# Kernel optimization log

Measured on AMD Instinct MI355X. Metric: run time of the kernel, lower is better.

Reference implementation:

```python
import jax, jax.numpy as jnp
import numpy as np

D_MODEL, D_STATE, D_CONV, EXPAND = 1024, 16, 4, 2
D_INNER = EXPAND * D_MODEL            # 2048
DT_RANK = int(np.ceil(D_MODEL / 16))  # 64
B, L = 2, 2048


def _dt_bias(key):
    # matches torch init: dt ~ exp(U(log dt_min, log dt_max)), inv via softplus inverse
    dt = jnp.exp(jax.random.uniform(key, (D_INNER,)) * (np.log(0.1) - np.log(0.001)) + np.log(0.001))
    dt = jnp.clip(dt, 1e-4, None)
    return dt + jnp.log(-jnp.expm1(-dt))


def _A_log():
    return jnp.log(jnp.tile(jnp.arange(1, D_STATE + 1, dtype=jnp.float32)[None, :], (D_INNER, 1)))


def setup_inputs() -> dict:
    key = jax.random.key(0)
    ks = jax.random.split(key, 16)
    n = lambda k, shape, s=0.02: jax.random.normal(k, shape, jnp.float32) * s
    return {
        "hidden_states": jax.random.normal(ks[0], (B, L, D_MODEL), jnp.float32),
        "in_proj_w": n(ks[1], (2 * D_INNER, D_MODEL)),
        "conv_w": n(ks[2], (D_INNER, 1, D_CONV), 0.2),
        "conv_b": jnp.zeros((D_INNER,), jnp.float32),
        "x_proj_w": n(ks[3], (DT_RANK + 2 * D_STATE, D_INNER)),
        "dt_proj_w": n(ks[4], (D_INNER, DT_RANK), 0.1),
        "dt_proj_b": _dt_bias(ks[5]),
        "A_log": _A_log(),
        "D": jnp.ones((D_INNER,), jnp.float32),
        "conv_w_b": n(ks[6], (D_INNER, 1, D_CONV), 0.2),
        "conv_b_b": jnp.zeros((D_INNER,), jnp.float32),
        "x_proj_w_b": n(ks[7], (DT_RANK + 2 * D_STATE, D_INNER)),
        "dt_proj_w_b": n(ks[8], (D_INNER, DT_RANK), 0.1),
        "dt_proj_b_b": _dt_bias(ks[9]),
        "A_b_log": _A_log(),
        "D_b": jnp.ones((D_INNER,), jnp.float32),
        "out_proj_w": n(ks[10], (D_MODEL, D_INNER)),
    }


def _silu(x):
    return x * jax.nn.sigmoid(x)


def _causal_dw_conv(x, w, b):
    # x: (B, Di, L); w: (Di, 1, K) depthwise; left-pad K-1 => causal, output length L
    y = jax.lax.conv_general_dilated(
        x, w, window_strides=(1,), padding=[(D_CONV - 1, 0)],
        dimension_numbers=("NCH", "OIH", "NCH"), feature_group_count=x.shape[1])
    return y + b[None, :, None]


def _mamba_branch(xz, conv_w, conv_b, x_proj_w, dt_proj_w, dt_proj_b, A_log, Dp):
    # xz: (B, 2*Di, L) -> y: (B, Di, L); selective scan (mamba_inner_fn_no_out_proj)
    x, z = jnp.split(xz, 2, axis=1)
    x = _silu(_causal_dw_conv(x, conv_w, conv_b))                       # (B,Di,L)
    x_dbl = jnp.einsum('rd,bdl->brl', x_proj_w, x)
    dt_r, Bc, Cc = jnp.split(x_dbl, [DT_RANK, DT_RANK + D_STATE], axis=1)
    delta = jax.nn.softplus(jnp.einsum('dr,brl->bdl', dt_proj_w, dt_r) + dt_proj_b[None, :, None])
    A = -jnp.exp(A_log)                                                 # (Di,N)

    def step(h, inp):
        d_t, u_t, b_t, c_t = inp   # (B,Di),(B,Di),(B,N),(B,N)
        h = h * jnp.exp(d_t[..., None] * A) + (d_t * u_t)[..., None] * b_t[:, None, :]
        return h, jnp.einsum('bdn,bn->bd', h, c_t)

    h0 = jnp.zeros((x.shape[0], D_INNER, D_STATE), x.dtype)
    xs = (jnp.moveaxis(delta, 2, 0), jnp.moveaxis(x, 2, 0),
          jnp.moveaxis(Bc, 2, 0), jnp.moveaxis(Cc, 2, 0))
    _, ys = jax.lax.scan(step, h0, xs)                                  # (L,B,Di)
    y = jnp.moveaxis(ys, 0, 2) + x * Dp[None, :, None]
    return y * _silu(z)


def reference(hidden_states, in_proj_w, conv_w, conv_b, x_proj_w, dt_proj_w, dt_proj_b,
              A_log, D, conv_w_b, conv_b_b, x_proj_w_b, dt_proj_w_b, dt_proj_b_b,
              A_b_log, D_b, out_proj_w):
    # bimamba_type == 'v2': forward scan + flipped backward scan, summed, then out_proj (no biases)
    xz = jnp.einsum('ed,bld->bel', in_proj_w, hidden_states)            # (B, 2*Di, L)
    out_f = _mamba_branch(xz, conv_w, conv_b, x_proj_w, dt_proj_w, dt_proj_b, A_log, D)
    out_r = _mamba_branch(xz[..., ::-1], conv_w_b, conv_b_b, x_proj_w_b,
                          dt_proj_w_b, dt_proj_b_b, A_b_log, D_b)[..., ::-1]
    y = out_f + out_r                                                   # (B,Di,L)
    return jnp.einsum('me,bel->blm', out_proj_w, y)                     # (B,L,D)
```

## Files before the change

kernel.cpp:

```cpp
#include <hip/hip_runtime.h>
#include <hip/hip_bf16.h>
#include <math.h>


#define L_SEQ  2048
#define B_SZ   2
#define DM     1024
#define DI     2048
#define NST    16
#define RTOT   96
#define DTR    64
#define NTOT   (B_SZ * L_SEQ)
#define ETOT   (2 * DI)
#define SPLK   8
#define CHTMAX 64

#define LOG2E  1.44269504088896340736f

#define OFF_X    ((size_t)0)
#define OFF_ZT   (OFF_X   + (size_t)DI * NTOT)
#define OFF_XCF  (OFF_ZT  + (size_t)DI * NTOT)
#define OFF_XCB  (OFF_XCF + (size_t)DI * NTOT)
#define OFF_DLTB (OFF_XCB + (size_t)DI * NTOT)
#define OFF_XDF  (OFF_DLTB + (size_t)DI * NTOT)
#define OFF_XDB  (OFF_XDF + (size_t)RTOT * NTOT)
#define OFF_SS   (OFF_XDB + (size_t)RTOT * NTOT)
#define OFF_HL   (OFF_SS  + (size_t)4 * 32 * DI)
#define OFF_YGTF (OFF_HL  + (size_t)4 * 32 * NST * DI)
#define OFF_YGTB (OFF_YGTF + (size_t)NTOT * DI / 2)
#define OFF_XDT16F (OFF_YGTB + (size_t)NTOT * DI / 2)
#define OFF_XDT16B (OFF_XDT16F + (size_t)NTOT * DTR / 2)
#define OFF_DTW16F (OFF_XDT16B + (size_t)NTOT * DTR / 2)
#define OFF_DTW16B (OFF_DTW16F + (size_t)DI * DTR / 2)
#define WS_FLOATS  (OFF_DTW16B + (size_t)DI * DTR / 2)
#define WS64_FLOATS (WS_FLOATS + (size_t)4 * 64 * DI + (size_t)4 * 64 * NST * DI)

typedef __bf16 bf16x8 __attribute__((ext_vector_type(8)));
typedef float  floatx4 __attribute__((ext_vector_type(4)));

__device__ __forceinline__ float silu_f(float x) {
    return x / (1.f + __expf(-x));
}

__device__ __forceinline__ void gl2lds16(const __bf16* g, __bf16* l) {
    __builtin_amdgcn_global_load_lds(
        (const __attribute__((address_space(1))) unsigned int*)g,
        (__attribute__((address_space(3))) unsigned int*)l, 16, 0, 0);
}

template<int MT, bool TRANS, bool SPLITZ>
__global__ __launch_bounds__(256)
void gemm_bf16(const __bf16* __restrict__ A, const __bf16* __restrict__ B,
               float* __restrict__ C, float* __restrict__ C2,
               int M, int N, int K)
{
    static_assert(MT == 64 || MT == 128, "vmcnt literals assume MT in {64,128}");
    __shared__ __attribute__((aligned(16))) __bf16 As[2][MT * 32];
    __shared__ __attribute__((aligned(16))) __bf16 Bs[2][128 * 32];
    const int tid  = threadIdx.x;
    const int m0   = blockIdx.y * MT;
    const int n0   = blockIdx.x * 128;
    const int lane = tid & 63;
    const int wave = tid >> 6;
    const int wy   = wave >> 1, wx = wave & 1;
    const int lr   = lane & 15;
    const int q    = lane >> 4;
    constexpr int MF = MT / 32;

    floatx4 acc[MF][4];
#pragma unroll
    for (int i = 0; i < MF; ++i)
#pragma unroll
        for (int j = 0; j < 4; ++j) acc[i][j] = (floatx4)(0.0f);

    const int rl = lane >> 2;
    const int cp = lane & 3;
    const int sw = (q ^ ((lr >> 2) & 3)) * 8;

    auto stage = [&](int s, int k0) {
#pragma unroll
        for (int is = 0; is < MT / 64; ++is) {
            int r0  = wave * (MT / 4) + is * 16;
            int row = r0 + rl;
            int c   = cp ^ ((row >> 2) & 3);
            gl2lds16(A + (size_t)(m0 + row) * K + k0 + c * 8, &As[s][r0 * 32]);
        }
#pragma unroll
        for (int is = 0; is < 2; ++is) {
            int r0  = wave * 32 + is * 16;
            int row = r0 + rl;
            int c   = cp ^ ((row >> 2) & 3);
            gl2lds16(B + (size_t)(n0 + row) * K + k0 + c * 8, &Bs[s][r0 * 32]);
        }
    };

    stage(0, 0);
    int cur = 0;
    for (int k0 = 0; k0 < K; k0 += 32) {
        if (k0 + 32 < K) {
            stage(cur ^ 1, k0 + 32);
            if constexpr (MT == 128) {
                asm volatile("s_waitcnt vmcnt(4)" ::: "memory");
            } else {
                asm volatile("s_waitcnt vmcnt(3)" ::: "memory");
            }
        } else {
            asm volatile("s_waitcnt vmcnt(0)" ::: "memory");
        }
        __builtin_amdgcn_s_barrier();

        bf16x8 af[MF], bfr[4];
#pragma unroll
        for (int i = 0; i < MF; ++i)
            af[i] = *(const bf16x8*)&As[cur][(wy * (MT / 2) + i * 16 + lr) * 32 + sw];
#pragma unroll
        for (int j = 0; j < 4; ++j)
            bfr[j] = *(const bf16x8*)&Bs[cur][(wx * 64 + j * 16 + lr) * 32 + sw];
#pragma unroll
        for (int i = 0; i < MF; ++i)
#pragma unroll
            for (int j = 0; j < 4; ++j)
                acc[i][j] = __builtin_amdgcn_mfma_f32_16x16x32_bf16(
                    af[i], bfr[j], acc[i][j], 0, 0, 0);
        __builtin_amdgcn_s_barrier();
        cur ^= 1;
    }

    const int mb = m0 + wy * (MT / 2);
    const int nb = n0 + wx * 64;
#pragma unroll
    for (int i = 0; i < MF; ++i) {
#pragma unroll
        for (int j = 0; j < 4; ++j) {
            int gn  = nb + j * 16 + lr;
            int gm0 = mb + i * 16 + q * 4;
            if constexpr (SPLITZ) {
                if (m0 < DI) {
#pragma unroll
                    for (int r = 0; r < 4; ++r)
                        C[(size_t)(gm0 + r) * N + gn] = acc[i][j][r];
                } else {
                    *(floatx4*)&C2[(size_t)gn * DI + (gm0 - DI)] = acc[i][j];
                }
            } else if constexpr (TRANS) {
                *(floatx4*)&C[(size_t)gn * M + gm0] = acc[i][j];
            } else {
#pragma unroll
                for (int r = 0; r < 4; ++r)
                    C[(size_t)(gm0 + r) * N + gn] = acc[i][j][r];
            }
        }
    }
}

__global__ __launch_bounds__(256)
void dtproj_mfma(const __bf16* __restrict__ Af, const __bf16* __restrict__ Ab,
                 const __bf16* __restrict__ Bwf, const __bf16* __restrict__ Bwb,
                 const float* __restrict__ bif, const float* __restrict__ bib,
                 float* __restrict__ outf, float* __restrict__ outb)
{
    __shared__ __attribute__((aligned(16))) __bf16 As[2][128 * 32];
    __shared__ __attribute__((aligned(16))) __bf16 Bs[2][128 * 32];
    const int br = blockIdx.z;
    const __bf16* A  = br ? Ab : Af;
    const __bf16* B  = br ? Bwb : Bwf;
    const float*  bi = br ? bib : bif;
    float*        C  = br ? outb : outf;

    const int tid  = threadIdx.x;
    const int m0   = blockIdx.y * 128;
    const int n0   = blockIdx.x * 128;
    const int lane = tid & 63;
    const int wave = tid >> 6;
    const int wy   = wave >> 1, wx = wave & 1;
    const int lr   = lane & 15;
    const int q    = lane >> 4;

    floatx4 acc[4][4];
#pragma unroll
    for (int i = 0; i < 4; ++i)
#pragma unroll
        for (int j = 0; j < 4; ++j) acc[i][j] = (floatx4)(0.0f);

    const int rl = lane >> 2;
    const int cp = lane & 3;
    const int sw = (q ^ ((lr >> 2) & 3)) * 8;

#pragma unroll
    for (int t = 0; t < 2; ++t) {
        int k0 = t * 32;
#pragma unroll
        for (int is = 0; is < 2; ++is) {
            int r0  = wave * 32 + is * 16;
            int row = r0 + rl;
            int c   = cp ^ ((row >> 2) & 3);
            gl2lds16(A + (size_t)(m0 + row) * DTR + k0 + c * 8, &As[t][r0 * 32]);
            gl2lds16(B + (size_t)(n0 + row) * DTR + k0 + c * 8, &Bs[t][r0 * 32]);
        }
    }

#pragma unroll
    for (int t = 0; t < 2; ++t) {
        if (t == 0) asm volatile("s_waitcnt vmcnt(4)" ::: "memory");
        else        asm volatile("s_waitcnt vmcnt(0)" ::: "memory");
        __builtin_amdgcn_s_barrier();

        bf16x8 af[4], bfr[4];
#pragma unroll
        for (int i = 0; i < 4; ++i)
            af[i] = *(const bf16x8*)&As[t][(wy * 64 + i * 16 + lr) * 32 + sw];
#pragma unroll
        for (int j = 0; j < 4; ++j)
            bfr[j] = *(const bf16x8*)&Bs[t][(wx * 64 + j * 16 + lr) * 32 + sw];
#pragma unroll
        for (int i = 0; i < 4; ++i)
#pragma unroll
            for (int j = 0; j < 4; ++j)
                acc[i][j] = __builtin_amdgcn_mfma_f32_16x16x32_bf16(
                    af[i], bfr[j], acc[i][j], 0, 0, 0);
    }

    const int mb = m0 + wy * 64;
    const int nb = n0 + wx * 64;
    float bj[4];
#pragma unroll
    for (int j = 0; j < 4; ++j) bj[j] = bi[nb + j * 16 + lr];
#pragma unroll
    for (int i = 0; i < 4; ++i) {
#pragma unroll
        for (int r = 0; r < 4; ++r) {
            int gm = mb + i * 16 + q * 4 + r;
#pragma unroll
            for (int j = 0; j < 4; ++j) {
                int gn = nb + j * 16 + lr;
                float x = acc[i][j][r] + bj[j];
                float o = (x > 20.f) ? x : __logf(1.f + __expf(x));
                C[(size_t)gm * DI + gn] = o;
            }
        }
    }
}

__global__ __launch_bounds__(256)
void cvt_bf16_k(const float* __restrict__ in, __bf16* __restrict__ out)
{
    const size_t i = ((size_t)blockIdx.x * 256 + threadIdx.x) * 8;
    float4 a = *(const float4*)(in + i);
    float4 b = *(const float4*)(in + i + 4);
    bf16x8 p;
    p[0]=(__bf16)a.x; p[1]=(__bf16)a.y; p[2]=(__bf16)a.z; p[3]=(__bf16)a.w;
    p[4]=(__bf16)b.x; p[5]=(__bf16)b.y; p[6]=(__bf16)b.z; p[7]=(__bf16)b.w;
    *(bf16x8*)(out + i) = p;
}

__global__ __launch_bounds__(256)
void addbf16_k(const __bf16* __restrict__ a, const __bf16* __restrict__ b,
               __bf16* __restrict__ o)
{
    const size_t i = ((size_t)blockIdx.x * 256 + threadIdx.x) * 8;
    bf16x8 x = *(const bf16x8*)(a + i);
    bf16x8 y = *(const bf16x8*)(b + i);
    bf16x8 s;
#pragma unroll
    for (int e = 0; e < 8; ++e) s[e] = (__bf16)((float)x[e] + (float)y[e]);
    *(bf16x8*)(o + i) = s;
}

__global__ __launch_bounds__(256)
void gemm_k3(const float* __restrict__ A, const float* __restrict__ Bm,
             float* __restrict__ C, int M, int N, int K)
{
    __shared__ float As[16][132];
    __shared__ float Bs[16][132];
    const int tid = threadIdx.x;
    const int n0 = blockIdx.x * 128;
    const int m0 = blockIdx.y * 128;
    int ksz  = K / (int)gridDim.z;
    int kbeg = blockIdx.z * ksz;
    int kend = kbeg + ksz;
    C += (size_t)blockIdx.z * M * N;
    const int tx = tid & 15, ty = tid >> 4;

    float acc[8][8];
#pragma unroll
    for (int i = 0; i < 8; ++i)
#pragma unroll
        for (int j = 0; j < 8; ++j) acc[i][j] = 0.f;

    for (int k0 = kbeg; k0 < kend; k0 += 16) {
#pragma unroll
        for (int it = 0; it < 2; ++it) {
            int i = tid + it * 256;
            int m = i >> 2, kq = i & 3;
            float4 v = make_float4(0.f, 0.f, 0.f, 0.f);
            int gm = m0 + m;
            if (gm < M) v = *(const float4*)(A + (size_t)gm * K + (k0 + kq * 4));
            As[kq * 4 + 0][m] = v.x; As[kq * 4 + 1][m] = v.y;
            As[kq * 4 + 2][m] = v.z; As[kq * 4 + 3][m] = v.w;
        }
#pragma unroll
        for (int it = 0; it < 2; ++it) {
            int i = tid + it * 256;
            int n = i >> 2, kq = i & 3;
            float4 v = *(const float4*)(Bm + (size_t)(n0 + n) * K + (k0 + kq * 4));
            Bs[kq * 4 + 0][n] = v.x; Bs[kq * 4 + 1][n] = v.y;
            Bs[kq * 4 + 2][n] = v.z; Bs[kq * 4 + 3][n] = v.w;
        }
        __syncthreads();
#pragma unroll
        for (int kk = 0; kk < 16; ++kk) {
            float av[8], bv[8];
            *(float4*)&av[0] = *(const float4*)&As[kk][ty * 8];
            *(float4*)&av[4] = *(const float4*)&As[kk][ty * 8 + 4];
            *(float4*)&bv[0] = *(const float4*)&Bs[kk][tx * 8];
            *(float4*)&bv[4] = *(const float4*)&Bs[kk][tx * 8 + 4];
#pragma unroll
            for (int i = 0; i < 8; ++i)
#pragma unroll
                for (int j = 0; j < 8; ++j)
                    acc[i][j] = fmaf(av[i], bv[j], acc[i][j]);
        }
        __syncthreads();
    }

#pragma unroll
    for (int i = 0; i < 8; ++i) {
        int gm = m0 + ty * 8 + i;
        if (gm < M) {
            float* cp = C + (size_t)gm * N + n0 + tx * 8;
            *(float4*)cp       = make_float4(acc[i][0], acc[i][1], acc[i][2], acc[i][3]);
            *(float4*)(cp + 4) = make_float4(acc[i][4], acc[i][5], acc[i][6], acc[i][7]);
        }
    }
}

__global__ __launch_bounds__(256)
void reduce8t_k(const float* __restrict__ P, float* __restrict__ out,
                __bf16* __restrict__ out2, size_t stride)
{
    const size_t i4 = ((size_t)blockIdx.x * 256 + threadIdx.x) * 4;
    float4 s = *(const float4*)(P + i4);
#pragma unroll
    for (int z = 1; z < SPLK; ++z) {
        float4 v = *(const float4*)(P + (size_t)z * stride + i4);
        s.x += v.x; s.y += v.y; s.z += v.z; s.w += v.w;
    }
    *(float4*)(out + i4) = s;
    const int r = (int)(i4 >> 12);
    if (r < DTR) {
        const int n = (int)(i4 & (NTOT - 1));
        out2[(size_t)(n + 0) * DTR + r] = (__bf16)s.x;
        out2[(size_t)(n + 1) * DTR + r] = (__bf16)s.y;
        out2[(size_t)(n + 2) * DTR + r] = (__bf16)s.z;
        out2[(size_t)(n + 3) * DTR + r] = (__bf16)s.w;
    }
}

__global__ __launch_bounds__(256)
void conv_k(const float* __restrict__ x,
            const float* __restrict__ wf, const float* __restrict__ bf,
            const float* __restrict__ wb, const float* __restrict__ bb,
            float* __restrict__ xcf, float* __restrict__ xcb)
{
    __shared__ float xs[70 * 65];
    const int tid = threadIdx.x;
    const int d0 = blockIdx.x * 64;
    const int n0 = blockIdx.y * 64;
    const int b  = n0 >> 11;
    const int l0 = n0 & (L_SEQ - 1);
    const size_t bbase = (size_t)b << 11;

    for (int i = tid; i < 64 * 70; i += 256) {
        int r = i / 70, c = i % 70;
        int l = l0 - 3 + c;
        float v = 0.f;
        if (l >= 0 && l < L_SEQ) v = x[(size_t)(d0 + r) * NTOT + bbase + l];
        xs[c * 65 + r] = v;
    }
    __syncthreads();

    const int dd = tid & 63;
    const int lq = tid >> 6;
    const int d  = d0 + dd;
    const float w0 = wf[d * 4 + 0], w1 = wf[d * 4 + 1];
    const float w2 = wf[d * 4 + 2], w3 = wf[d * 4 + 3];
    const float v0 = wb[d * 4 + 0], v1 = wb[d * 4 + 1];
    const float v2 = wb[d * 4 + 2], v3 = wb[d * 4 + 3];
    const float bfv = bf[d], bbv = bb[d];

    for (int lr = 0; lr < 64; lr += 4) {
        const int lo = lr + lq;
        const int l  = l0 + lo;
        float x0 = xs[(lo + 0) * 65 + dd];
        float x1 = xs[(lo + 1) * 65 + dd];
        float x2 = xs[(lo + 2) * 65 + dd];
        float x3 = xs[(lo + 3) * 65 + dd];
        float x4 = xs[(lo + 4) * 65 + dd];
        float x5 = xs[(lo + 5) * 65 + dd];
        float x6 = xs[(lo + 6) * 65 + dd];
        float xf = bfv + w0 * x0 + w1 * x1 + w2 * x2 + w3 * x3;
        xcf[((size_t)bbase + l) * DI + d] = silu_f(xf);
        float xb = bbv + v3 * x3 + v2 * x4 + v1 * x5 + v0 * x6;
        xcb[((size_t)bbase + (L_SEQ - 1 - l)) * DI + d] = silu_f(xb);
    }
}

__global__ __launch_bounds__(256)
void scan_part1(const float* __restrict__ xcf, const float* __restrict__ xcb,
                const float* __restrict__ xdf, const float* __restrict__ xdb,
                const float* __restrict__ dltf, const float* __restrict__ dltb,
                const float* __restrict__ Alog_f, const float* __restrict__ Alog_b,
                float* __restrict__ SS, float* __restrict__ HL,
                int nch, int csh)
{
    __shared__ float Bsh[NST][CHTMAX];
    const int cht = 1 << csh;
    const int tid = threadIdx.x;
    const int d  = blockIdx.x * 256 + tid;
    const int c  = blockIdx.y;
    const int bb = blockIdx.z;
    const int b  = bb & 1;
    const int br = bb >> 1;

    const float* u    = br ? xcb : xcf;
    const float* dl   = br ? dltb : dltf;
    const float* xd   = br ? xdb : xdf;
    const float* Alog = br ? Alog_b : Alog_f;

    const size_t nbase = (size_t)b * L_SEQ + (size_t)c * cht;
    const float* bcB = xd + (size_t)DTR * NTOT + nbase;

    for (int i = tid; i < NST * cht; i += 256) {
        int n = i >> csh;
        int t = i & (cht - 1);
        Bsh[n][t] = bcB[(size_t)n * NTOT + t];
    }

    float Arow[NST], h[NST];
#pragma unroll
    for (int n = 0; n < NST; ++n) {
        Arow[n] = -__expf(Alog[d * NST + n]) * LOG2E;
        h[n] = 0.f;
    }
    float S = 0.f;

    const float* up = u  + nbase * DI + d;
    const float* dp = dl + nbase * DI + d;

    __syncthreads();

    float dva[4], uva[4], dvb[4], uvb[4];
#pragma unroll
    for (int k = 0; k < 4; ++k) {
        dva[k] = dp[(size_t)k * DI];
        uva[k] = up[(size_t)k * DI];
    }
#pragma unroll
    for (int k = 0; k < 4; ++k) {
        dvb[k] = dp[(size_t)(4 + k) * DI];
        uvb[k] = up[(size_t)(4 + k) * DI];
    }

    for (int tr = 0; tr < cht; tr += 4) {
        float dvn[4], uvn[4];
#pragma unroll
        for (int k = 0; k < 4; ++k) {
            dvn[k] = dp[(size_t)(tr + 8 + k) * DI];
            uvn[k] = up[(size_t)(tr + 8 + k) * DI];
        }
        S += (dva[0] + dva[1]) + (dva[2] + dva[3]);
        float du[4] = { dva[0]*uva[0], dva[1]*uva[1], dva[2]*uva[2], dva[3]*uva[3] };
#pragma unroll
        for (int n = 0; n < NST; ++n) {
            float4 Bn = *(const float4*)&Bsh[n][tr];
            float hn = h[n];
            float An = Arow[n];
            hn = hn * __builtin_amdgcn_exp2f(dva[0] * An) + du[0] * Bn.x;
            hn = hn * __builtin_amdgcn_exp2f(dva[1] * An) + du[1] * Bn.y;
            hn = hn * __builtin_amdgcn_exp2f(dva[2] * An) + du[2] * Bn.z;
            hn = hn * __builtin_amdgcn_exp2f(dva[3] * An) + du[3] * Bn.w;
            h[n] = hn;
        }
#pragma unroll
        for (int k = 0; k < 4; ++k) {
            dva[k] = dvb[k]; uva[k] = uvb[k];
            dvb[k] = dvn[k]; uvb[k] = uvn[k];
        }
    }
    SS[((size_t)bb * nch + c) * DI + d] = S;
#pragma unroll
    for (int n = 0; n < NST; ++n)
        HL[(((size_t)bb * nch + c) * NST + n) * DI + d] = h[n];
}

__global__ __launch_bounds__(256)
void scan_part2(const float* __restrict__ SS, float* HL,
                const float* __restrict__ Alog_f, const float* __restrict__ Alog_b,
                int nch)
{
    const int d  = blockIdx.x * 256 + threadIdx.x;
    const int n  = blockIdx.y;
    const int bb = blockIdx.z;
    const int br = bb >> 1;
    const float* Alog = br ? Alog_b : Alog_f;
    const float A = -__expf(Alog[d * NST + n]) * LOG2E;

    float H = 0.f;
    for (int c = 0; c < nch; ++c) {
        const size_t si = ((size_t)bb * nch + c) * DI + d;
        const size_t hi = (((size_t)bb * nch + c) * NST + n) * DI + d;
        float hl = HL[hi];
        HL[hi] = H;
        H = __builtin_amdgcn_exp2f(SS[si] * A) * H + hl;
    }
}

__global__ __launch_bounds__(256)
void scan_part3(const float* __restrict__ zt,
                const float* __restrict__ xcf, const float* __restrict__ xcb,
                const float* __restrict__ xdf, const float* __restrict__ xdb,
                const float* __restrict__ dltf, const float* __restrict__ dltb,
                const float* __restrict__ HIN,
                __bf16* __restrict__ ygtf, __bf16* __restrict__ ygtb,
                const float* __restrict__ Alog_f, const float* __restrict__ Alog_b,
                const float* __restrict__ Df, const float* __restrict__ Db,
                int nch, int csh)
{
    __shared__ float BCs[2 * NST][CHTMAX];
    const int cht = 1 << csh;
    const int tid = threadIdx.x;
    const int d  = blockIdx.x * 256 + tid;
    const int c  = blockIdx.y;
    const int bb = blockIdx.z;
    const int b  = bb & 1;
    const int br = bb >> 1;

    const float* u    = br ? xcb : xcf;
    const float* dl   = br ? dltb : dltf;
    const float* xd   = br ? xdb : xdf;
    const float* Alog = br ? Alog_b : Alog_f;
    const float* Dv   = br ? Db : Df;
    __bf16*      ygt  = br ? ygtb : ygtf;

    const size_t nbase = (size_t)b * L_SEQ + (size_t)c * cht;
    const float* bcB = xd + (size_t)DTR * NTOT + nbase;

    for (int i = tid; i < 2 * NST * cht; i += 256) {
        int n = i >> csh;
        int t = i & (cht - 1);
        BCs[n][t] = bcB[(size_t)n * NTOT + t];
    }

    float Arow[NST], h[NST];
#pragma unroll
    for (int n = 0; n < NST; ++n) {
        Arow[n] = -__expf(Alog[d * NST + n]) * LOG2E;
        h[n] = HIN[(((size_t)bb * nch + c) * NST + n) * DI + d];
    }
    const float Dp = Dv[d];

    const float* up = u  + nbase * DI + d;
    const float* dp = dl + nbase * DI + d;
    const int    bL = b * L_SEQ;
    const int    t0 = c * cht;

    __syncthreads();

    float dva[4], uva[4], dvb[4], uvb[4];
#pragma unroll
    for (int k = 0; k < 4; ++k) {
        dva[k] = dp[(size_t)k * DI];
        uva[k] = up[(size_t)k * DI];
    }
#pragma unroll
    for (int k = 0; k < 4; ++k) {
        dvb[k] = dp[(size_t)(4 + k) * DI];
        uvb[k] = up[(size_t)(4 + k) * DI];
    }
    int   ncur[4];
    float zcur[4];
#pragma unroll
    for (int k = 0; k < 4; ++k) {
        int t = t0 + k;
        ncur[k] = br ? (bL + (L_SEQ - 1 - t)) : (bL + t);
        zcur[k] = zt[(ptrdiff_t)ncur[k] * DI + d];
    }

    for (int tr = 0; tr < cht; tr += 4) {
        float dvn[4], uvn[4], znx[4];
        int   nnx[4];
#pragma unroll
        for (int k = 0; k < 4; ++k) {
            dvn[k] = dp[(size_t)(tr + 8 + k) * DI];
            uvn[k] = up[(size_t)(tr + 8 + k) * DI];
        }
#pragma unroll
        for (int k = 0; k < 4; ++k) {
            int t = t0 + tr + 4 + k;
            nnx[k] = br ? (bL + (L_SEQ - 1 - t)) : (bL + t);
            znx[k] = zt[(ptrdiff_t)nnx[k] * DI + d];
        }

        float du[4] = { dva[0]*uva[0], dva[1]*uva[1], dva[2]*uva[2], dva[3]*uva[3] };
        float y[4] = { 0.f, 0.f, 0.f, 0.f };
#pragma unroll
        for (int n = 0; n < NST; ++n) {
            float4 Bn = *(const float4*)&BCs[n][tr];
            float4 Cn = *(const float4*)&BCs[NST + n][tr];
            float hn = h[n];
            float An = Arow[n];
            hn = hn * __builtin_amdgcn_exp2f(dva[0] * An) + du[0] * Bn.x;  y[0] = fmaf(hn, Cn.x, y[0]);
            hn = hn * __builtin_amdgcn_exp2f(dva[1] * An) + du[1] * Bn.y;  y[1] = fmaf(hn, Cn.y, y[1]);
            hn = hn * __builtin_amdgcn_exp2f(dva[2] * An) + du[2] * Bn.z;  y[2] = fmaf(hn, Cn.z, y[2]);
            hn = hn * __builtin_amdgcn_exp2f(dva[3] * An) + du[3] * Bn.w;  y[3] = fmaf(hn, Cn.w, y[3]);
            h[n] = hn;
        }
#pragma unroll
        for (int k = 0; k < 4; ++k) {
            float yo = (y[k] + uva[k] * Dp) * silu_f(zcur[k]);
            ygt[(size_t)ncur[k] * DI + d] = (__bf16)yo;
        }
#pragma unroll
        for (int k = 0; k < 4; ++k) {
            dva[k] = dvb[k]; uva[k] = uvb[k];
            dvb[k] = dvn[k]; uvb[k] = uvn[k];
            ncur[k] = nnx[k]; zcur[k] = znx[k];
        }
    }
}

extern "C" void kernel_launch(void* const* d_in, const int* in_sizes, int n_in,
                              void* d_out, int out_size, void* d_ws, size_t ws_size,
                              hipStream_t stream)
{
    const float* hid     = (const float*)d_in[0];
    const float* inw     = (const float*)d_in[1];
    const float* convw   = (const float*)d_in[2];
    const float* convb   = (const float*)d_in[3];
    const float* xpw     = (const float*)d_in[4];
    const float* dtw     = (const float*)d_in[5];
    const float* dtb     = (const float*)d_in[6];
    const float* Alog    = (const float*)d_in[7];
    const float* Dv      = (const float*)d_in[8];
    const float* convw_b = (const float*)d_in[9];
    const float* convb_b = (const float*)d_in[10];
    const float* xpw_b   = (const float*)d_in[11];
    const float* dtw_b   = (const float*)d_in[12];
    const float* dtb_b   = (const float*)d_in[13];
    const float* Alog_b  = (const float*)d_in[14];
    const float* Dv_b    = (const float*)d_in[15];
    const float* outw    = (const float*)d_in[16];
    float* out = (float*)d_out;
    float* ws  = (float*)d_ws;

    if (ws_size < WS_FLOATS * sizeof(float)) return;

    const bool big = ws_size >= WS64_FLOATS * sizeof(float);
    const int  nch = big ? 64 : 32;
    const int  csh = big ? 5 : 6;

    float*  X    = ws + OFF_X;
    float*  ZT   = ws + OFF_ZT;
    float*  XCF  = ws + OFF_XCF;
    float*  XCB  = ws + OFF_XCB;
    float*  DLTB = ws + OFF_DLTB;
    float*  XDF  = ws + OFF_XDF;
    float*  XDB  = ws + OFF_XDB;
    float*  SS   = big ? (ws + WS_FLOATS) : (ws + OFF_SS);
    float*  HLb  = SS + (size_t)4 * nch * DI;
    __bf16* YGTF = (__bf16*)(ws + OFF_YGTF);
    __bf16* YGTB = (__bf16*)(ws + OFF_YGTB);
    float*  PF   = ws + OFF_YGTF;
    float*  PB   = ws + OFF_YGTB;
    float*  DLTF = X;
    __bf16* IW16 = (__bf16*)(ws + OFF_SS);
    __bf16* HD16 = IW16 + (size_t)ETOT * DM;
    __bf16* OW16 = (__bf16*)(ws + OFF_XCB);
    __bf16* YGS  = (__bf16*)(ws + OFF_XCF);
    __bf16* XDT16F = (__bf16*)(ws + OFF_XDT16F);
    __bf16* XDT16B = (__bf16*)(ws + OFF_XDT16B);
    __bf16* DTW16F = (__bf16*)(ws + OFF_DTW16F);
    __bf16* DTW16B = (__bf16*)(ws + OFF_DTW16B);

    dim3 blk(256);
    cvt_bf16_k<<<dim3(ETOT * DM / 2048), blk, 0, stream>>>(inw, IW16);
    cvt_bf16_k<<<dim3(NTOT * DM / 2048), blk, 0, stream>>>(hid, HD16);
    cvt_bf16_k<<<dim3(DI * DTR / 2048), blk, 0, stream>>>(dtw, DTW16F);
    cvt_bf16_k<<<dim3(DI * DTR / 2048), blk, 0, stream>>>(dtw_b, DTW16B);
    gemm_bf16<128, false, true><<<dim3(32, 32), blk, 0, stream>>>(
        IW16, HD16, X, ZT, ETOT, NTOT, DM);
    conv_k<<<dim3(32, 64), blk, 0, stream>>>(X, convw, convb, convw_b, convb_b, XCF, XCB);
    gemm_k3<<<dim3(32, 1, SPLK), blk, 0, stream>>>(xpw, XCF, PF, RTOT, NTOT, DI);
    gemm_k3<<<dim3(32, 1, SPLK), blk, 0, stream>>>(xpw_b, XCB, PB, RTOT, NTOT, DI);
    reduce8t_k<<<dim3(RTOT * NTOT / 1024), blk, 0, stream>>>(PF, XDF, XDT16F, (size_t)RTOT * NTOT);
    reduce8t_k<<<dim3(RTOT * NTOT / 1024), blk, 0, stream>>>(PB, XDB, XDT16B, (size_t)RTOT * NTOT);
    dtproj_mfma<<<dim3(DI / 128, NTOT / 128, 2), blk, 0, stream>>>(
        XDT16F, XDT16B, DTW16F, DTW16B, dtb, dtb_b, DLTF, DLTB);
    scan_part1<<<dim3(DI / 256, nch, 4), blk, 0, stream>>>(
        XCF, XCB, XDF, XDB, DLTF, DLTB, Alog, Alog_b, SS, HLb, nch, csh);
    scan_part2<<<dim3(DI / 256, NST, 4), blk, 0, stream>>>(
        SS, HLb, Alog, Alog_b, nch);
    scan_part3<<<dim3(DI / 256, nch, 4), blk, 0, stream>>>(
        ZT, XCF, XCB, XDF, XDB, DLTF, DLTB, HLb, YGTF, YGTB, Alog, Alog_b, Dv, Dv_b,
        nch, csh);
    cvt_bf16_k<<<dim3(DM * DI / 2048), blk, 0, stream>>>(outw, OW16);
    addbf16_k<<<dim3(NTOT * DI / 2048), blk, 0, stream>>>(YGTF, YGTB, YGS);
    gemm_bf16<64, true, false><<<dim3(32, 16), blk, 0, stream>>>(
        OW16, YGS, out, nullptr, DM, NTOT, DI);

    (void)in_sizes; (void)n_in; (void)out_size;
}
```

Before: 479.0 us.

## Move SiLU gate into branch-sum kernel and batch paired launches

The z gate is factored out of both scan branches, since (y_f + y_b) * silu(z) equals the sum of the separately gated outputs. The scan kernel now stores ungated y, and the bf16 add kernel reads z once and applies the gate. This avoids reading z twice and removes silu work and index bookkeeping from the scan inner loop. Separately, the forward/backward conversion, x_proj GEMM and reduce launches are merged into single launches selected by a grid dimension, cutting launch count. One side effect is that bf16 rounding now happens before gating, which slightly changes numerics.

```diff
diff --git a/kernel.cpp b/kernel.cpp
--- a/kernel.cpp
+++ b/kernel.cpp
@@ -242,8 +242,11 @@
 }
 
 __global__ __launch_bounds__(256)
-void cvt_bf16_k(const float* __restrict__ in, __bf16* __restrict__ out)
-{
+void cvt2_bf16_k(const float* __restrict__ ia, __bf16* __restrict__ oa,
+                 const float* __restrict__ ib, __bf16* __restrict__ ob)
+{
+    const float* in  = blockIdx.y ? ib : ia;
+    __bf16*      out = blockIdx.y ? ob : oa;
     const size_t i = ((size_t)blockIdx.x * 256 + threadIdx.x) * 8;
     float4 a = *(const float4*)(in + i);
     float4 b = *(const float4*)(in + i + 4);
@@ -254,31 +257,55 @@
 }
 
 __global__ __launch_bounds__(256)
-void addbf16_k(const __bf16* __restrict__ a, const __bf16* __restrict__ b,
-               __bf16* __restrict__ o)
+void cvt_bf16_k(const float* __restrict__ in, __bf16* __restrict__ out)
+{
+    const size_t i = ((size_t)blockIdx.x * 256 + threadIdx.x) * 8;
+    float4 a = *(const float4*)(in + i);
+    float4 b = *(const float4*)(in + i + 4);
+    bf16x8 p;
+    p[0]=(__bf16)a.x; p[1]=(__bf16)a.y; p[2]=(__bf16)a.z; p[3]=(__bf16)a.w;
+    p[4]=(__bf16)b.x; p[5]=(__bf16)b.y; p[6]=(__bf16)b.z; p[7]=(__bf16)b.w;
+    *(bf16x8*)(out + i) = p;
+}
+
+__global__ __launch_bounds__(256)
+void gatesum_k(const __bf16* __restrict__ a, const __bf16* __restrict__ b,
+               const float* __restrict__ z, __bf16* __restrict__ o)
 {
     const size_t i = ((size_t)blockIdx.x * 256 + threadIdx.x) * 8;
     bf16x8 x = *(const bf16x8*)(a + i);
     bf16x8 y = *(const bf16x8*)(b + i);
+    float4 z0 = *(const float4*)(z + i);
+    float4 z1 = *(const float4*)(z + i + 4);
+    float zz[8] = { z0.x, z0.y, z0.z, z0.w, z1.x, z1.y, z1.z, z1.w };
     bf16x8 s;
 #pragma unroll
-    for (int e = 0; e < 8; ++e) s[e] = (__bf16)((float)x[e] + (float)y[e]);
+    for (int e = 0; e < 8; ++e)
+        s[e] = (__bf16)(((float)x[e] + (float)y[e]) * silu_f(zz[e]));
     *(bf16x8*)(o + i) = s;
 }
 
 __global__ __launch_bounds__(256)
-void gemm_k3(const float* __restrict__ A, const float* __restrict__ Bm,
-             float* __restrict__ C, int M, int N, int K)
+void gemm_k3(const float* __restrict__ Af, const float* __restrict__ Bmf,
+             float* __restrict__ Cf,
+             const float* __restrict__ Ab, const float* __restrict__ Bmb,
+             float* __restrict__ Cb,
+             int M, int N, int K)
 {
     __shared__ float As[16][132];
     __shared__ float Bs[16][132];
     const int tid = threadIdx.x;
     const int n0 = blockIdx.x * 128;
     const int m0 = blockIdx.y * 128;
-    int ksz  = K / (int)gridDim.z;
-    int kbeg = blockIdx.z * ksz;
+    const int zz = blockIdx.z;
+    const int brc = (zz >= SPLK) ? 1 : 0;
+    const int kz  = zz & (SPLK - 1);
+    const float* A  = brc ? Ab : Af;
+    const float* Bm = brc ? Bmb : Bmf;
+    float* C = (brc ? Cb : Cf) + (size_t)kz * M * N;
+    int ksz  = K / SPLK;
+    int kbeg = kz * ksz;
     int kend = kbeg + ksz;
-    C += (size_t)blockIdx.z * M * N;
     const int tx = tid & 15, ty = tid >> 4;
 
     float acc[8][8];
@@ -335,9 +362,14 @@
 }
 
 __global__ __launch_bounds__(256)
-void reduce8t_k(const float* __restrict__ P, float* __restrict__ out,
-                __bf16* __restrict__ out2, size_t stride)
-{
+void reduce8t_k(const float* __restrict__ Pf, float* __restrict__ outf,
+                __bf16* __restrict__ out2f,
+                const float* __restrict__ Pb, float* __restrict__ outb,
+                __bf16* __restrict__ out2b, size_t stride)
+{
+    const float* P   = blockIdx.y ? Pb : Pf;
+    float*      outp = blockIdx.y ? outb : outf;
+    __bf16*     out2 = blockIdx.y ? out2b : out2f;
     const size_t i4 = ((size_t)blockIdx.x * 256 + threadIdx.x) * 4;
     float4 s = *(const float4*)(P + i4);
 #pragma unroll
@@ -345,7 +377,7 @@
         float4 v = *(const float4*)(P + (size_t)z * stride + i4);
         s.x += v.x; s.y += v.y; s.z += v.z; s.w += v.w;
     }
-    *(float4*)(out + i4) = s;
+    *(float4*)(outp + i4) = s;
     const int r = (int)(i4 >> 12);
     if (r < DTR) {
         const int n = (int)(i4 & (NTOT - 1));
@@ -516,8 +548,7 @@
 }
 
 __global__ __launch_bounds__(256)
-void scan_part3(const float* __restrict__ zt,
-                const float* __restrict__ xcf, const float* __restrict__ xcb,
+void scan_part3(const float* __restrict__ xcf, const float* __restrict__ xcb,
                 const float* __restrict__ xdf, const float* __restrict__ xdb,
                 const float* __restrict__ dltf, const float* __restrict__ dltb,
                 const float* __restrict__ HIN,
@@ -577,28 +608,13 @@
         dvb[k] = dp[(size_t)(4 + k) * DI];
         uvb[k] = up[(size_t)(4 + k) * DI];
     }
-    int   ncur[4];
-    float zcur[4];
-#pragma unroll
-    for (int k = 0; k < 4; ++k) {
-        int t = t0 + k;
-        ncur[k] = br ? (bL + (L_SEQ - 1 - t)) : (bL + t);
-        zcur[k] = zt[(ptrdiff_t)ncur[k] * DI + d];
-    }
 
     for (int tr = 0; tr < cht; tr += 4) {
-        float dvn[4], uvn[4], znx[4];
-        int   nnx[4];
+        float dvn[4], uvn[4];
 #pragma unroll
         for (int k = 0; k < 4; ++k) {
             dvn[k] = dp[(size_t)(tr + 8 + k) * DI];
             uvn[k] = up[(size_t)(tr + 8 + k) * DI];
-        }
-#pragma unroll
-        for (int k = 0; k < 4; ++k) {
-            int t = t0 + tr + 4 + k;
-            nnx[k] = br ? (bL + (L_SEQ - 1 - t)) : (bL + t);
-            znx[k] = zt[(ptrdiff_t)nnx[k] * DI + d];
         }
 
         float du[4] = { dva[0]*uva[0], dva[1]*uva[1], dva[2]*uva[2], dva[3]*uva[3] };
@@ -617,14 +633,14 @@
         }
 #pragma unroll
         for (int k = 0; k < 4; ++k) {
-            float yo = (y[k] + uva[k] * Dp) * silu_f(zcur[k]);
-            ygt[(size_t)ncur[k] * DI + d] = (__bf16)yo;
+            int t = t0 + tr + k;
+            int nn = br ? (bL + (L_SEQ - 1 - t)) : (bL + t);
+            ygt[(size_t)nn * DI + d] = (__bf16)(y[k] + uva[k] * Dp);
         }
 #pragma unroll
         for (int k = 0; k < 4; ++k) {
             dva[k] = dvb[k]; uva[k] = uvb[k];
             dvb[k] = dvn[k]; uvb[k] = uvn[k];
-            ncur[k] = nnx[k]; zcur[k] = znx[k];
         }
     }
 }
@@ -683,17 +699,15 @@
     __bf16* DTW16B = (__bf16*)(ws + OFF_DTW16B);
 
     dim3 blk(256);
-    cvt_bf16_k<<<dim3(ETOT * DM / 2048), blk, 0, stream>>>(inw, IW16);
-    cvt_bf16_k<<<dim3(NTOT * DM / 2048), blk, 0, stream>>>(hid, HD16);
-    cvt_bf16_k<<<dim3(DI * DTR / 2048), blk, 0, stream>>>(dtw, DTW16F);
-    cvt_bf16_k<<<dim3(DI * DTR / 2048), blk, 0, stream>>>(dtw_b, DTW16B);
+    cvt2_bf16_k<<<dim3(ETOT * DM / 2048, 2), blk, 0, stream>>>(inw, IW16, hid, HD16);
+    cvt2_bf16_k<<<dim3(DI * DTR / 2048, 2), blk, 0, stream>>>(dtw, DTW16F, dtw_b, DTW16B);
     gemm_bf16<128, false, true><<<dim3(32, 32), blk, 0, stream>>>(
         IW16, HD16, X, ZT, ETOT, NTOT, DM);
     conv_k<<<dim3(32, 64), blk, 0, stream>>>(X, convw, convb, convw_b, convb_b, XCF, XCB);
-    gemm_k3<<<dim3(32, 1, SPLK), blk, 0, stream>>>(xpw, XCF, PF, RTOT, NTOT, DI);
-    gemm_k3<<<dim3(32, 1, SPLK), blk, 0, stream>>>(xpw_b, XCB, PB, RTOT, NTOT, DI);
-    reduce8t_k<<<dim3(RTOT * NTOT / 1024), blk, 0, stream>>>(PF, XDF, XDT16F, (size_t)RTOT * NTOT);
-    reduce8t_k<<<dim3(RTOT * NTOT / 1024), blk, 0, stream>>>(PB, XDB, XDT16B, (size_t)RTOT * NTOT);
+    gemm_k3<<<dim3(32, 1, 2 * SPLK), blk, 0, stream>>>(
+        xpw, XCF, PF, xpw_b, XCB, PB, RTOT, NTOT, DI);
+    reduce8t_k<<<dim3(RTOT * NTOT / 1024, 2), blk, 0, stream>>>(
+        PF, XDF, XDT16F, PB, XDB, XDT16B, (size_t)RTOT * NTOT);
     dtproj_mfma<<<dim3(DI / 128, NTOT / 128, 2), blk, 0, stream>>>(
         XDT16F, XDT16B, DTW16F, DTW16B, dtb, dtb_b, DLTF, DLTB);
     scan_part1<<<dim3(DI / 256, nch, 4), blk, 0, stream>>>(
@@ -701,10 +715,10 @@
     scan_part2<<<dim3(DI / 256, NST, 4), blk, 0, stream>>>(
         SS, HLb, Alog, Alog_b, nch);
     scan_part3<<<dim3(DI / 256, nch, 4), blk, 0, stream>>>(
-        ZT, XCF, XCB, XDF, XDB, DLTF, DLTB, HLb, YGTF, YGTB, Alog, Alog_b, Dv, Dv_b,
+        XCF, XCB, XDF, XDB, DLTF, DLTB, HLb, YGTF, YGTB, Alog, Alog_b, Dv, Dv_b,
         nch, csh);
     cvt_bf16_k<<<dim3(DM * DI / 2048), blk, 0, stream>>>(outw, OW16);
-    addbf16_k<<<dim3(NTOT * DI / 2048), blk, 0, stream>>>(YGTF, YGTB, YGS);
+    gatesum_k<<<dim3(NTOT * DI / 2048), blk, 0, stream>>>(YGTF, YGTB, ZT, YGS);
     gemm_bf16<64, true, false><<<dim3(32, 16), blk, 0, stream>>>(
         OW16, YGS, out, nullptr, DM, NTOT, DI);
 
```

Result: faster. 437.3 us (-8.7%).
